# Kernel optimization log

Measured on AMD Instinct MI355X. Metric: run time of the kernel, lower is better.

## Reference

```python
import jax, jax.numpy as jnp
import numpy as np

B, F, D, A, T = 16384, 128, 256, 256, 64  # batch, num_features, token_dim, att_dim, num_tokens
DECAY = 0.9  # 1.0 - accumulator_decay(0.1)


def setup_inputs() -> dict:
    key = jax.random.key(0)
    ks = jax.random.split(key, 16)
    s = lambda k, shape, fan: jax.random.normal(k, shape, jnp.float32) / np.sqrt(fan)
    return {
        "features": jax.random.normal(ks[0], (B, F), jnp.float32),
        "h": jax.random.normal(ks[1], (B, D), jnp.float32),
        "accumulator": jax.random.normal(ks[2], (B, D), jnp.float32),
        "mask": jax.random.bernoulli(ks[3], 0.5, (B,)),
        "tokens": jax.random.normal(ks[4], (T, D), jnp.float32),
        # GRUCell params (torch layout: gates ordered r,z,n)
        "W_ih": s(ks[5], (3 * D, F), F),
        "W_hh": s(ks[6], (3 * D, D), D),
        "b_ih": s(ks[7], (3 * D,), D),
        "b_hh": s(ks[8], (3 * D,), D),
        # Additive attention params
        "Wh": s(ks[9], (A, D), D),
        "bh": s(ks[10], (A,), D),
        "Wc": s(ks[11], (A, D), D),
        "bc": s(ks[12], (A,), D),
        "v": s(ks[13], (A,), A),
        "bv": s(ks[14], (1,), A),
    }


def gru_cell(x, h, W_ih, W_hh, b_ih, b_hh):
    gi = x @ W_ih.T + b_ih          # [B, 3D]
    gh = h @ W_hh.T + b_hh          # [B, 3D]
    i_r, i_z, i_n = jnp.split(gi, 3, axis=-1)
    h_r, h_z, h_n = jnp.split(gh, 3, axis=-1)
    r = jax.nn.sigmoid(i_r + h_r)
    z = jax.nn.sigmoid(i_z + h_z)
    n = jnp.tanh(i_n + r * h_n)
    return (1.0 - z) * n + z * h


def reference(features, h, accumulator, mask, tokens,
              W_ih, W_hh, b_ih, b_hh, Wh, bh, Wc, bc, v, bv):
    # GRU step computed densely; masked rows selected afterwards (same math as
    # the original boolean-mask gather -> GRUCell -> scatter chain).
    h_new = gru_cell(features, h, W_ih, W_hh, b_ih, b_hh)        # [B, D]
    h_out = jnp.where(mask[:, None], h_new, h)

    # Additive attention over tanh(tokens) with context h_new.
    hist = jnp.tanh(tokens)                                       # [T, D] (shared across batch)
    tok_proj = hist @ Wh.T + bh                                   # [T, A]
    ctx_proj = h_new @ Wc.T + bc                                  # [B, A]
    e = jnp.tanh(tok_proj[None, :, :] + ctx_proj[:, None, :])     # [B, T, A]
    scores = jnp.einsum("bta,a->bt", e, v) + bv                  # [B, T]
    weights = jax.nn.softmax(scores, axis=-1)                     # [B, T]
    emb = jnp.einsum("bt,td->bd", weights, hist)                 # [B, D]

    # Decayed accumulator update, only on masked rows.
    emb_out = jnp.where(mask[:, None], accumulator * DECAY + emb, accumulator)
    return emb_out, h_out
```

## Files before the change

### kernel.cpp

```cpp
#include <hip/hip_runtime.h>
#include <hip/hip_bf16.h>

#define B_ 16384
#define F_ 128
#define D_ 256
#define A_ 256
#define T_ 64
#define DECAY_ 0.9f
#define SCALE2 2.885390081777927f
#define L2E    1.4426950408889634f

typedef __attribute__((ext_vector_type(8))) __bf16 bf16x8;
typedef __attribute__((ext_vector_type(4))) float f32x4;

#if __has_builtin(__builtin_amdgcn_exp2f)
#define EXP2(x) __builtin_amdgcn_exp2f(x)
#else
#define EXP2(x) exp2f(x)
#endif
#define RCP(x) __builtin_amdgcn_rcpf(x)

__device__ __forceinline__ float tanh2(float x) {
    float e = EXP2(SCALE2 * x);
    return 1.0f - 2.0f * RCP(e + 1.0f);
}
__device__ __forceinline__ float sigmoid2(float x) {
    float e = EXP2(-L2E * x);
    return RCP(1.0f + e);
}
__device__ __forceinline__ bool get_mask(const void* mp, int mflag, int row) {
    if (mflag) return ((const unsigned char*)mp)[row] != 0;
    return ((const int*)mp)[row] != 0;
}
__device__ __forceinline__ unsigned short bfbits(float f) {
    __bf16 h = (__bf16)f;
    return __builtin_bit_cast(unsigned short, h);
}
__device__ __forceinline__ float bits2f(unsigned short u) {
    return __builtin_bit_cast(float, ((unsigned)u) << 16);
}

__global__ __launch_bounds__(256) void convert_prep(
    const float* Wih, const float* Whh, const float* Wc,
    __bf16* Wihb, __bf16* Whhb, __bf16* Wcb,
    const unsigned int* mword, int* flag,
    const float* tokens, const float* Wh, const float* bh,
    __bf16* histT, __bf16* etp)
{
    __shared__ float hrow[D_];
    const int n1 = 768 * 128, n2 = n1 + 768 * 256, n3 = n2 + 256 * 256;
    int bid = blockIdx.x;
    int tid = threadIdx.x;

    if (bid >= 353) {
        int t = bid - 353;
        float hv = tanh2(tokens[t * D_ + tid]);
        hrow[tid] = hv;
        histT[tid * T_ + t] = (__bf16)hv;
        __syncthreads();
        float acc = bh[tid];
        const float* wr = &Wh[tid * D_];
        for (int d = 0; d < D_; d++) acc += hrow[d] * wr[d];
        etp[(tid >> 2) * 256 + t * 4 + (tid & 3)] = (__bf16)EXP2(acc * SCALE2);
        return;
    }
    if (bid == 352) {
        __shared__ int f;
        if (tid == 0) f = 0;
        __syncthreads();
        int any = 0;
        for (int i = tid; i < B_ / 4; i += 256) any |= (mword[i] > 1u) ? 1 : 0;
        if (any) atomicOr(&f, 1);
        __syncthreads();
        if (tid == 0) flag[0] = f;
        return;
    }
    int i = (bid * 256 + tid) * 4;
    if (i < n1) {
#pragma unroll
        for (int j = 0; j < 4; ++j) Wihb[i + j] = (__bf16)Wih[i + j];
    } else if (i < n2) {
        int k = i - n1;
#pragma unroll
        for (int j = 0; j < 4; ++j) Whhb[k + j] = (__bf16)Whh[k + j];
    } else if (i < n3) {
        int k = i - n2;
#pragma unroll
        for (int j = 0; j < 4; ++j) Wcb[k + j] = (__bf16)Wc[k + j];
    }
}

#define XS 392
__global__ __launch_bounds__(1024) void gru_fused(
    const float* __restrict__ features, const float* __restrict__ h,
    const void* maskp, const int* __restrict__ mflagp,
    const __bf16* __restrict__ Wihb, const __bf16* __restrict__ Whhb, const __bf16* __restrict__ Wcb,
    const float* __restrict__ b_ih, const float* __restrict__ b_hh, const float* __restrict__ bcp,
    float* __restrict__ hout, __bf16* __restrict__ ecb)
{
    __shared__ __bf16 Xs[64 * XS];
    int tid = threadIdx.x;
    int b0 = blockIdx.x * 64;
    int wv = tid >> 6, lane = tid & 63;
    int lan15 = lane & 15, kg = lane >> 4;
    int klo = kg * 8;
    int d = wv * 16 + lan15;
    int mflag = mflagp[0];

#pragma unroll
    for (int it = 0; it < 2; ++it) {
        int idx = (it * 1024 + tid) * 4;
        int r = idx >> 7, c = idx & 127;
        float4 vv = *(const float4*)&features[(size_t)(b0 + r) * F_ + c];
        ushort4 w = { bfbits(vv.x), bfbits(vv.y), bfbits(vv.z), bfbits(vv.w) };
        *reinterpret_cast<ushort4*>(&Xs[r * XS + c]) = w;
    }
#pragma unroll
    for (int it = 0; it < 4; ++it) {
        int idx = (it * 1024 + tid) * 4;
        int r = idx >> 8, c = idx & 255;
        float4 vv = *(const float4*)&h[(size_t)(b0 + r) * D_ + c];
        ushort4 w = { bfbits(vv.x), bfbits(vv.y), bfbits(vv.z), bfbits(vv.w) };
        *reinterpret_cast<ushort4*>(&Xs[r * XS + 128 + c]) = w;
    }
    float brv = b_ih[d] + b_hh[d];
    float bzv = b_ih[256 + d] + b_hh[256 + d];
    float biv = b_ih[512 + d];
    float bhv = b_hh[512 + d];
    float bcv = bcp[d];
    __syncthreads();

    f32x4 ar[4] = {}, az[4] = {}, ai[4] = {}, ah[4] = {};

#pragma unroll
    for (int kb = 0; kb < 4; ++kb) {
        bf16x8 a[4];
#pragma unroll
        for (int rf = 0; rf < 4; ++rf)
            a[rf] = *reinterpret_cast<const bf16x8*>(&Xs[(rf * 16 + lan15) * XS + kb * 32 + klo]);
        const __bf16* p = Wihb + (size_t)d * F_ + kb * 32 + klo;
        bf16x8 br = *reinterpret_cast<const bf16x8*>(p);
        bf16x8 bz = *reinterpret_cast<const bf16x8*>(p + 256 * F_);
        bf16x8 bn = *reinterpret_cast<const bf16x8*>(p + 512 * F_);
#pragma unroll
        for (int rf = 0; rf < 4; ++rf) {
            ar[rf] = __builtin_amdgcn_mfma_f32_16x16x32_bf16(a[rf], br, ar[rf], 0, 0, 0);
            az[rf] = __builtin_amdgcn_mfma_f32_16x16x32_bf16(a[rf], bz, az[rf], 0, 0, 0);
            ai[rf] = __builtin_amdgcn_mfma_f32_16x16x32_bf16(a[rf], bn, ai[rf], 0, 0, 0);
        }
    }
#pragma unroll
    for (int kb = 0; kb < 8; ++kb) {
        bf16x8 a[4];
#pragma unroll
        for (int rf = 0; rf < 4; ++rf)
            a[rf] = *reinterpret_cast<const bf16x8*>(&Xs[(rf * 16 + lan15) * XS + 128 + kb * 32 + klo]);
        const __bf16* p = Whhb + (size_t)d * D_ + kb * 32 + klo;
        bf16x8 br = *reinterpret_cast<const bf16x8*>(p);
        bf16x8 bz = *reinterpret_cast<const bf16x8*>(p + 256 * D_);
        bf16x8 bn = *reinterpret_cast<const bf16x8*>(p + 512 * D_);
#pragma unroll
        for (int rf = 0; rf < 4; ++rf) {
            ar[rf] = __builtin_amdgcn_mfma_f32_16x16x32_bf16(a[rf], br, ar[rf], 0, 0, 0);
            az[rf] = __builtin_amdgcn_mfma_f32_16x16x32_bf16(a[rf], bz, az[rf], 0, 0, 0);
            ah[rf] = __builtin_amdgcn_mfma_f32_16x16x32_bf16(a[rf], bn, ah[rf], 0, 0, 0);
        }
    }

    __syncthreads();

#pragma unroll
    for (int rf = 0; rf < 4; ++rf) {
#pragma unroll
        for (int rg = 0; rg < 4; ++rg) {
            int row = rf * 16 + kg * 4 + rg;
            int grow = b0 + row;
            float hv = (float)Xs[row * XS + 128 + d];
            float rv = sigmoid2(ar[rf][rg] + brv);
            float zv = sigmoid2(az[rf][rg] + bzv);
            float nv = tanh2(ai[rf][rg] + biv + rv * (ah[rf][rg] + bhv));
            float hn = (1.0f - zv) * nv + zv * hv;
            Xs[row * XS + 128 + d] = (__bf16)hn;
            bool m = get_mask(maskp, mflag, grow);
            hout[(size_t)grow * D_ + d] = m ? hn : hv;
        }
    }
    __syncthreads();

    f32x4 ac[4] = {};
#pragma unroll
    for (int kb = 0; kb < 8; ++kb) {
        bf16x8 b = *reinterpret_cast<const bf16x8*>(&Wcb[(size_t)d * D_ + kb * 32 + klo]);
#pragma unroll
        for (int rf = 0; rf < 4; ++rf) {
            bf16x8 a = *reinterpret_cast<const bf16x8*>(&Xs[(rf * 16 + lan15) * XS + 128 + kb * 32 + klo]);
            ac[rf] = __builtin_amdgcn_mfma_f32_16x16x32_bf16(a, b, ac[rf], 0, 0, 0);
        }
    }
#pragma unroll
    for (int rf = 0; rf < 4; ++rf) {
#pragma unroll
        for (int rg = 0; rg < 4; ++rg) {
            int row = rf * 16 + kg * 4 + rg;
            ecb[(size_t)(b0 + row) * A_ + d] = (__bf16)EXP2((ac[rf][rg] + bcv) * SCALE2);
        }
    }
}

__global__ __launch_bounds__(256) void attn11(
    const __bf16* __restrict__ ecb_g, const unsigned short* __restrict__ etp,
    const __bf16* __restrict__ histT, const float* __restrict__ v,
    const float* __restrict__ accum, const void* maskp, const int* __restrict__ mflagp,
    float* __restrict__ out_emb)
{
    __shared__ float ecs[16 * A_];
    __shared__ float vs[A_];
    __shared__ __bf16 wgtb[16 * 72];
    int tid = threadIdx.x;
    int b0 = blockIdx.x * 16;
    int wv = tid >> 6, lane = tid & 63;
    int mflag = mflagp[0];

    {
        const bf16x8* src = (const bf16x8*)(ecb_g + (size_t)b0 * A_);
#pragma unroll
        for (int it = 0; it < 2; ++it) {
            int e = it * 256 + tid;
            bf16x8 w8 = src[e];
            float4 lo, hi;
            lo.x = (float)w8[0]; lo.y = (float)w8[1]; lo.z = (float)w8[2]; lo.w = (float)w8[3];
            hi.x = (float)w8[4]; hi.y = (float)w8[5]; hi.z = (float)w8[6]; hi.w = (float)w8[7];
            *(float4*)&ecs[e * 8] = lo;
            *(float4*)&ecs[e * 8 + 4] = hi;
        }
        if (tid < 64) ((float4*)vs)[tid] = ((const float4*)v)[tid];
    }
    __syncthreads();

    const float* ecb = ecs + (size_t)(wv * 4) * A_;

    float p0 = 0.f, p1 = 0.f, p2 = 0.f, p3 = 0.f;
#pragma unroll 4
    for (int ch = 0; ch < 32; ++ch) {
        int a0 = ch * 8;
        const unsigned short* ep = etp + (a0 >> 2) * 256 + lane * 4;
        uint2 q0 = *(const uint2*)ep;
        uint2 q1 = *(const uint2*)(ep + 256);
        float4 vA = *(const float4*)&vs[a0];
        float4 vB = *(const float4*)&vs[a0 + 4];
        float ecr[4][8];
#pragma unroll
        for (int r = 0; r < 4; ++r) {
            float4 ca = *(const float4*)&ecb[r * A_ + a0];
            float4 cb = *(const float4*)&ecb[r * A_ + a0 + 4];
            ecr[r][0] = ca.x; ecr[r][1] = ca.y; ecr[r][2] = ca.z; ecr[r][3] = ca.w;
            ecr[r][4] = cb.x; ecr[r][5] = cb.y; ecr[r][6] = cb.z; ecr[r][7] = cb.w;
        }
        float et[8];
        et[0] = __builtin_bit_cast(float, q0.x << 16);
        et[1] = __builtin_bit_cast(float, q0.x & 0xffff0000u);
        et[2] = __builtin_bit_cast(float, q0.y << 16);
        et[3] = __builtin_bit_cast(float, q0.y & 0xffff0000u);
        et[4] = __builtin_bit_cast(float, q1.x << 16);
        et[5] = __builtin_bit_cast(float, q1.x & 0xffff0000u);
        et[6] = __builtin_bit_cast(float, q1.y << 16);
        et[7] = __builtin_bit_cast(float, q1.y & 0xffff0000u);
        float vv[8];
        vv[0] = vA.x; vv[1] = vA.y; vv[2] = vA.z; vv[3] = vA.w;
        vv[4] = vB.x; vv[5] = vB.y; vv[6] = vB.z; vv[7] = vB.w;
#pragma unroll
        for (int j = 0; j < 8; ++j) {
            float s0 = RCP(fmaf(et[j], ecr[0][j], 1.0f));
            float s1 = RCP(fmaf(et[j], ecr[1][j], 1.0f));
            float s2 = RCP(fmaf(et[j], ecr[2][j], 1.0f));
            float s3 = RCP(fmaf(et[j], ecr[3][j], 1.0f));
            p0 = fmaf(vv[j], s0, p0);
            p1 = fmaf(vv[j], s1, p1);
            p2 = fmaf(vv[j], s2, p2);
            p3 = fmaf(vv[j], s3, p3);
        }
    }

    float xs[4] = { -2.0f * p0, -2.0f * p1, -2.0f * p2, -2.0f * p3 };
#pragma unroll
    for (int r = 0; r < 4; ++r) {
        float x = xs[r];
        float mx = x;
#pragma unroll
        for (int m = 1; m < 64; m <<= 1) mx = fmaxf(mx, __shfl_xor(mx, m, 64));
        float e = EXP2(L2E * (x - mx));
        float s = e;
#pragma unroll
        for (int m = 1; m < 64; m <<= 1) s += __shfl_xor(s, m, 64);
        wgtb[(wv * 4 + r) * 72 + lane] = (__bf16)(e * RCP(s));
    }
    __syncthreads();

    int lan15 = lane & 15, kg = lane >> 4, klo = kg * 8;
    f32x4 em[4] = {};
#pragma unroll
    for (int kb = 0; kb < 2; ++kb) {
        bf16x8 afrag = *reinterpret_cast<const bf16x8*>(&wgtb[lan15 * 72 + kb * 32 + klo]);
#pragma unroll
        for (int nt = 0; nt < 4; ++nt) {
            int n = wv * 64 + nt * 16 + lan15;
            bf16x8 bfrag = *reinterpret_cast<const bf16x8*>(&histT[n * T_ + kb * 32 + klo]);
            em[nt] = __builtin_amdgcn_mfma_f32_16x16x32_bf16(afrag, bfrag, em[nt], 0, 0, 0);
        }
    }
#pragma unroll
    for (int rg = 0; rg < 4; ++rg) {
        int row = kg * 4 + rg;
        size_t grow = (size_t)(b0 + row);
        bool m = get_mask(maskp, mflag, (int)grow);
#pragma unroll
        for (int nt = 0; nt < 4; ++nt) {
            int d = wv * 64 + nt * 16 + lan15;
            float av = accum[grow * D_ + d];
            out_emb[grow * D_ + d] = m ? fmaf(av, DECAY_, em[nt][rg]) : av;
        }
    }
}

extern "C" void kernel_launch(void* const* d_in, const int* in_sizes, int n_in,
                              void* d_out, int out_size, void* d_ws, size_t ws_size,
                              hipStream_t stream) {
    const float* features = (const float*)d_in[0];
    const float* h        = (const float*)d_in[1];
    const float* accum    = (const float*)d_in[2];
    const void*  maskp    = d_in[3];
    const float* tokens   = (const float*)d_in[4];
    const float* Wih      = (const float*)d_in[5];
    const float* Whh      = (const float*)d_in[6];
    const float* bih      = (const float*)d_in[7];
    const float* bhh      = (const float*)d_in[8];
    const float* Wh       = (const float*)d_in[9];
    const float* bh       = (const float*)d_in[10];
    const float* Wc       = (const float*)d_in[11];
    const float* bc       = (const float*)d_in[12];
    const float* v        = (const float*)d_in[13];

    float* out = (float*)d_out;

    __bf16* Wihb  = (__bf16*)d_ws;
    __bf16* Whhb  = Wihb + 768 * 128;
    __bf16* Wcb   = Whhb + 768 * 256;
    __bf16* histT = Wcb + 256 * 256;
    __bf16* etp   = histT + 256 * 64;
    __bf16* ecb   = etp + 64 * 256;
    int*    mflag = (int*)(ecb + (size_t)B_ * D_);

    hipLaunchKernelGGL(convert_prep, dim3(417), dim3(256), 0, stream,
                       Wih, Whh, Wc, Wihb, Whhb, Wcb,
                       (const unsigned int*)maskp, mflag,
                       tokens, Wh, bh, histT, etp);
    hipLaunchKernelGGL(gru_fused, dim3(B_ / 64), dim3(1024), 0, stream,
                       features, h, maskp, mflag, Wihb, Whhb, Wcb, bih, bhh, bc,
                       out + (size_t)B_ * D_, ecb);
    hipLaunchKernelGGL(attn11, dim3(B_ / 16), dim3(256), 0, stream,
                       ecb, (const unsigned short*)etp, histT, v, accum, maskp, mflag, out);
}
```

Before: 84.76 us.

## Fuse attention kernel into GRU kernel, keep context projection in LDS

Merges the separate attention kernel into the GRU kernel so the exponentiated context projection stays in shared memory as fp32 instead of being written to and reread from global memory as bf16. This removes one kernel launch and the round trip of a B×A intermediate buffer. Each 1024-thread block now handles 64 rows of attention with 16 waves, reusing the GRU staging LDS. The cost is a larger LDS footprint per block (64 KB plus extras), which may reduce occupancy, and the attention phase now runs with the GRU kernel's 1024-thread block shape.

```diff
diff --git a/kernel.cpp b/kernel.cpp
--- a/kernel.cpp
+++ b/kernel.cpp
@@ -35,9 +35,6 @@
 __device__ __forceinline__ unsigned short bfbits(float f) {
     __bf16 h = (__bf16)f;
     return __builtin_bit_cast(unsigned short, h);
-}
-__device__ __forceinline__ float bits2f(unsigned short u) {
-    return __builtin_bit_cast(float, ((unsigned)u) << 16);
 }
 
 __global__ __launch_bounds__(256) void convert_prep(
@@ -91,14 +88,20 @@
 }
 
 #define XS 392
-__global__ __launch_bounds__(1024) void gru_fused(
+__global__ __launch_bounds__(1024) void gru_attn(
     const float* __restrict__ features, const float* __restrict__ h,
     const void* maskp, const int* __restrict__ mflagp,
     const __bf16* __restrict__ Wihb, const __bf16* __restrict__ Whhb, const __bf16* __restrict__ Wcb,
     const float* __restrict__ b_ih, const float* __restrict__ b_hh, const float* __restrict__ bcp,
-    float* __restrict__ hout, __bf16* __restrict__ ecb)
+    const unsigned short* __restrict__ etp, const __bf16* __restrict__ histT,
+    const float* __restrict__ v, const float* __restrict__ accum,
+    float* __restrict__ hout, float* __restrict__ out_emb)
 {
-    __shared__ __bf16 Xs[64 * XS];
+    __shared__ __align__(16) unsigned char smem[64 * 256 * 4];
+    __bf16* Xs  = (__bf16*)smem;
+    float*  ecl = (float*)smem;
+    __shared__ float vs[A_];
+    __shared__ __bf16 wgtb[64 * 72];
     int tid = threadIdx.x;
     int b0 = blockIdx.x * 64;
     int wv = tid >> 6, lane = tid & 63;
@@ -123,6 +126,7 @@
         ushort4 w = { bfbits(vv.x), bfbits(vv.y), bfbits(vv.z), bfbits(vv.w) };
         *reinterpret_cast<ushort4*>(&Xs[r * XS + 128 + c]) = w;
     }
+    if (tid < 64) ((float4*)vs)[tid] = ((const float4*)v)[tid];
     float brv = b_ih[d] + b_hh[d];
     float bzv = b_ih[256 + d] + b_hh[256 + d];
     float biv = b_ih[512 + d];
@@ -131,7 +135,6 @@
     __syncthreads();
 
     f32x4 ar[4] = {}, az[4] = {}, ai[4] = {}, ah[4] = {};
-
 #pragma unroll
     for (int kb = 0; kb < 4; ++kb) {
         bf16x8 a[4];
@@ -166,7 +169,6 @@
             ah[rf] = __builtin_amdgcn_mfma_f32_16x16x32_bf16(a[rf], bn, ah[rf], 0, 0, 0);
         }
     }
-
     __syncthreads();
 
 #pragma unroll
@@ -197,48 +199,19 @@
             ac[rf] = __builtin_amdgcn_mfma_f32_16x16x32_bf16(a, b, ac[rf], 0, 0, 0);
         }
     }
+    __syncthreads();
+
 #pragma unroll
     for (int rf = 0; rf < 4; ++rf) {
 #pragma unroll
         for (int rg = 0; rg < 4; ++rg) {
             int row = rf * 16 + kg * 4 + rg;
-            ecb[(size_t)(b0 + row) * A_ + d] = (__bf16)EXP2((ac[rf][rg] + bcv) * SCALE2);
-        }
-    }
-}
-
-__global__ __launch_bounds__(256) void attn11(
-    const __bf16* __restrict__ ecb_g, const unsigned short* __restrict__ etp,
-    const __bf16* __restrict__ histT, const float* __restrict__ v,
-    const float* __restrict__ accum, const void* maskp, const int* __restrict__ mflagp,
-    float* __restrict__ out_emb)
-{
-    __shared__ float ecs[16 * A_];
-    __shared__ float vs[A_];
-    __shared__ __bf16 wgtb[16 * 72];
-    int tid = threadIdx.x;
-    int b0 = blockIdx.x * 16;
-    int wv = tid >> 6, lane = tid & 63;
-    int mflag = mflagp[0];
-
-    {
-        const bf16x8* src = (const bf16x8*)(ecb_g + (size_t)b0 * A_);
-#pragma unroll
-        for (int it = 0; it < 2; ++it) {
-            int e = it * 256 + tid;
-            bf16x8 w8 = src[e];
-            float4 lo, hi;
-            lo.x = (float)w8[0]; lo.y = (float)w8[1]; lo.z = (float)w8[2]; lo.w = (float)w8[3];
-            hi.x = (float)w8[4]; hi.y = (float)w8[5]; hi.z = (float)w8[6]; hi.w = (float)w8[7];
-            *(float4*)&ecs[e * 8] = lo;
-            *(float4*)&ecs[e * 8 + 4] = hi;
-        }
-        if (tid < 64) ((float4*)vs)[tid] = ((const float4*)v)[tid];
-    }
-    __syncthreads();
-
-    const float* ecb = ecs + (size_t)(wv * 4) * A_;
-
+            ecl[row * 256 + d] = EXP2((ac[rf][rg] + bcv) * SCALE2);
+        }
+    }
+    __syncthreads();
+
+    const float* ecb = ecl + (size_t)(wv * 4) * 256;
     float p0 = 0.f, p1 = 0.f, p2 = 0.f, p3 = 0.f;
 #pragma unroll 4
     for (int ch = 0; ch < 32; ++ch) {
@@ -251,8 +224,8 @@
         float ecr[4][8];
 #pragma unroll
         for (int r = 0; r < 4; ++r) {
-            float4 ca = *(const float4*)&ecb[r * A_ + a0];
-            float4 cb = *(const float4*)&ecb[r * A_ + a0 + 4];
+            float4 ca = *(const float4*)&ecb[r * 256 + a0];
+            float4 cb = *(const float4*)&ecb[r * 256 + a0 + 4];
             ecr[r][0] = ca.x; ecr[r][1] = ca.y; ecr[r][2] = ca.z; ecr[r][3] = ca.w;
             ecr[r][4] = cb.x; ecr[r][5] = cb.y; ecr[r][6] = cb.z; ecr[r][7] = cb.w;
         }
@@ -281,10 +254,10 @@
         }
     }
 
-    float xs[4] = { -2.0f * p0, -2.0f * p1, -2.0f * p2, -2.0f * p3 };
+    float xs4[4] = { -2.0f * p0, -2.0f * p1, -2.0f * p2, -2.0f * p3 };
 #pragma unroll
     for (int r = 0; r < 4; ++r) {
-        float x = xs[r];
+        float x = xs4[r];
         float mx = x;
 #pragma unroll
         for (int m = 1; m < 64; m <<= 1) mx = fmaxf(mx, __shfl_xor(mx, m, 64));
@@ -296,28 +269,28 @@
     }
     __syncthreads();
 
-    int lan15 = lane & 15, kg = lane >> 4, klo = kg * 8;
+    int rg4 = wv >> 2, cg = wv & 3;
     f32x4 em[4] = {};
 #pragma unroll
     for (int kb = 0; kb < 2; ++kb) {
-        bf16x8 afrag = *reinterpret_cast<const bf16x8*>(&wgtb[lan15 * 72 + kb * 32 + klo]);
+        bf16x8 afrag = *reinterpret_cast<const bf16x8*>(&wgtb[(rg4 * 16 + lan15) * 72 + kb * 32 + klo]);
 #pragma unroll
         for (int nt = 0; nt < 4; ++nt) {
-            int n = wv * 64 + nt * 16 + lan15;
+            int n = cg * 64 + nt * 16 + lan15;
             bf16x8 bfrag = *reinterpret_cast<const bf16x8*>(&histT[n * T_ + kb * 32 + klo]);
             em[nt] = __builtin_amdgcn_mfma_f32_16x16x32_bf16(afrag, bfrag, em[nt], 0, 0, 0);
         }
     }
 #pragma unroll
     for (int rg = 0; rg < 4; ++rg) {
-        int row = kg * 4 + rg;
+        int row = rg4 * 16 + kg * 4 + rg;
         size_t grow = (size_t)(b0 + row);
         bool m = get_mask(maskp, mflag, (int)grow);
 #pragma unroll
         for (int nt = 0; nt < 4; ++nt) {
-            int d = wv * 64 + nt * 16 + lan15;
-            float av = accum[grow * D_ + d];
-            out_emb[grow * D_ + d] = m ? fmaf(av, DECAY_, em[nt][rg]) : av;
+            int d2 = cg * 64 + nt * 16 + lan15;
+            float av = accum[grow * D_ + d2];
+            out_emb[grow * D_ + d2] = m ? fmaf(av, DECAY_, em[nt][rg]) : av;
         }
     }
 }
@@ -347,16 +320,14 @@
     __bf16* Wcb   = Whhb + 768 * 256;
     __bf16* histT = Wcb + 256 * 256;
     __bf16* etp   = histT + 256 * 64;
-    __bf16* ecb   = etp + 64 * 256;
-    int*    mflag = (int*)(ecb + (size_t)B_ * D_);
+    int*    mflag = (int*)(etp + 64 * 256);
 
     hipLaunchKernelGGL(convert_prep, dim3(417), dim3(256), 0, stream,
                        Wih, Whh, Wc, Wihb, Whhb, Wcb,
                        (const unsigned int*)maskp, mflag,
                        tokens, Wh, bh, histT, etp);
-    hipLaunchKernelGGL(gru_fused, dim3(B_ / 64), dim3(1024), 0, stream,
+    hipLaunchKernelGGL(gru_attn, dim3(B_ / 64), dim3(1024), 0, stream,
                        features, h, maskp, mflag, Wihb, Whhb, Wcb, bih, bhh, bc,
-                       out + (size_t)B_ * D_, ecb);
-    hipLaunchKernelGGL(attn11, dim3(B_ / 16), dim3(256), 0, stream,
-                       ecb, (const unsigned short*)etp, histT, v, accum, maskp, mflag, out);
-}
+                       (const unsigned short*)etp, histT, v, accum,
+                       out + (size_t)B_ * D_, out);
+}
```

Result: slower. 86.73 us (+2.3%).
